# Performance work log

Hardware: AMD Instinct MI355X
Metric: run time of the kernel (lower is better)

## Reference

```python
import jax, jax.numpy as jnp
import numpy as np

D = 16      # stroke_embedding_dim
H = 2       # num_heads
DH = D // H # head dim = 8
HID = 32    # hidden_dim
OUT = 32    # output_dim
N = 250000  # num edge nodes
F = 500000  # num faces
E = 4       # edges per face


def setup_inputs() -> dict:
    key = jax.random.key(0)
    ks = jax.random.split(key, 10)
    s = 1.0 / np.sqrt(D)
    return {
        "node_embed": jax.random.normal(ks[0], (1, N, D), dtype=jnp.float32),
        "face_edge_ids": jax.random.randint(ks[1], (F, E), 0, N),
        # nn.MultiheadAttention in_proj (packed q,k,v) and out_proj, stored [in, out]
        "w_in": jax.random.uniform(ks[2], (D, 3 * D), jnp.float32, -s, s),
        "b_in": jnp.zeros((3 * D,), jnp.float32),
        "w_out": jax.random.uniform(ks[3], (D, D), jnp.float32, -s, s),
        "b_out": jnp.zeros((D,), jnp.float32),
        # fc: Linear(16 -> 32), fc_output: Linear(32 -> 32)
        "fc_w": jax.random.uniform(ks[4], (D, HID), jnp.float32, -s, s),
        "fc_b": jax.random.uniform(ks[5], (HID,), jnp.float32, -s, s),
        "fco_w": jax.random.uniform(ks[6], (HID, OUT), jnp.float32, -1 / np.sqrt(HID), 1 / np.sqrt(HID)),
        "fco_b": jax.random.uniform(ks[7], (OUT,), jnp.float32, -1 / np.sqrt(HID), 1 / np.sqrt(HID)),
    }


def reference(node_embed, face_edge_ids, w_in, b_in, w_out, b_out, fc_w, fc_b, fco_w, fco_b):
    # Gather per-face edge embeddings: [F, E, D]
    x = node_embed[0][face_edge_ids]
    # Packed qkv projection
    qkv = x @ w_in + b_in                                  # [F, E, 3D]
    q, k, v = jnp.split(qkv, 3, axis=-1)
    def heads(t):
        return t.reshape(F, E, H, DH).transpose(0, 2, 1, 3)  # [F, H, E, DH]
    q, k, v = heads(q), heads(k), heads(v)
    scores = jnp.einsum("fhqd,fhkd->fhqk", q, k) / np.sqrt(DH)
    attn = jax.nn.softmax(scores, axis=-1)
    o = jnp.einsum("fhqk,fhkd->fhqd", attn, v)             # [F, H, E, DH]
    o = o.transpose(0, 2, 1, 3).reshape(F, E, D)
    attn_out = o @ w_out + b_out                           # [F, E, D]
    h = jax.nn.relu(attn_out @ fc_w + fc_b)                # [F, E, HID]
    pooled = h.mean(axis=1)                                # [F, HID]
    out = pooled @ fco_w + fco_b                           # [F, OUT]
    return out[None]                                       # [1, F, OUT]
```

## Files before the change

### kernel.cpp

```cpp
#include <hip/hip_runtime.h>
#include <stdint.h>


typedef _Float16 v2h __attribute__((ext_vector_type(2)));
typedef __fp16 h4 __attribute__((ext_vector_type(4)));
typedef float f32x4 __attribute__((ext_vector_type(4)));
typedef uint32_t u32x2 __attribute__((ext_vector_type(2)));

#define DPP_ROT1 0x39
#define DPP_ROT2 0x4E
#define DPP_ROT3 0x93

template<int CTRL>
static __device__ __forceinline__ float dppf(float x) {
    return __builtin_bit_cast(float,
        __builtin_amdgcn_mov_dpp(__builtin_bit_cast(int, x), CTRL, 0xF, 0xF, true));
}

static __device__ __forceinline__ v2h pkh(float a, float b) {
    v2h r; r.x = (_Float16)a; r.y = (_Float16)b; return r;
}
static __device__ __forceinline__ v2h pkrtz(float a, float b) {
#if __has_builtin(__builtin_amdgcn_cvt_pkrtz)
    return __builtin_bit_cast(v2h, __builtin_amdgcn_cvt_pkrtz(a, b));
#else
    return pkh(a, b);
#endif
}
static __device__ __forceinline__ uint32_t bcu(v2h h) {
    return __builtin_bit_cast(uint32_t, h);
}
static __device__ __forceinline__ h4 mkh4(uint32_t lo, uint32_t hi) {
    u32x2 t; t.x = lo; t.y = hi; return __builtin_bit_cast(h4, t);
}
static __device__ __forceinline__ h4 ld2h(const uint32_t* p) {
    u32x2 t; t.x = p[0]; t.y = p[1]; return __builtin_bit_cast(h4, t);
}
static __device__ __forceinline__ f32x4 mfma16(h4 a, h4 b, f32x4 c) {
    return __builtin_amdgcn_mfma_f32_16x16x16f16(a, b, c, 0, 0, 0);
}
static __device__ __forceinline__ h4 packC(f32x4 c) {
    return mkh4(bcu(pkrtz(c[0], c[1])), bcu(pkrtz(c[2], c[3])));
}
static __device__ __forceinline__ h4 packCrelu(f32x4 c) {
    return mkh4(bcu(pkrtz(fmaxf(c[0], 0.f), fmaxf(c[1], 0.f))),
                bcu(pkrtz(fmaxf(c[2], 0.f), fmaxf(c[3], 0.f))));
}
static __device__ __forceinline__ h4 selh(bool keep, h4 x) {
    u32x2 t = __builtin_bit_cast(u32x2, x);
    u32x2 r; r.x = keep ? t.x : 0u; r.y = keep ? t.y : 0u;
    return __builtin_bit_cast(h4, r);
}

__global__ void fold_w(const float* __restrict__ w_in,
                       const float* __restrict__ w_out,
                       const float* __restrict__ b_out,
                       const float* __restrict__ fc_w,
                       const float* __restrict__ fc_b,
                       const float* __restrict__ fco_w,
                       uint32_t* __restrict__ wsu) {
    const int tid = threadIdx.x;
    if (blockIdx.x == 0) {
        if (tid < 384) {
            const int T = tid >> 7, r = tid & 127, l = r >> 1, d = r & 1;
            const int o = 16 * T + (l & 15), k0 = 4 * (l >> 4) + 2 * d;
            wsu[tid] = bcu(pkh(w_in[k0 * 48 + o], w_in[(k0 + 1) * 48 + o]));
        } else if (tid < 640) {
            const int i = tid - 384, b = i >> 7, r = i & 127, l = r >> 1, d = r & 1;
            const int c = 16 * b + (l & 15), k0 = 4 * (l >> 4) + 2 * d;
            float a0 = 0.f, a1 = 0.f;
#pragma unroll
            for (int e = 0; e < 16; ++e) {
                a0 = fmaf(w_out[k0 * 16 + e],       fc_w[e * 32 + c], a0);
                a1 = fmaf(w_out[(k0 + 1) * 16 + e], fc_w[e * 32 + c], a1);
            }
            wsu[tid] = bcu(pkh(a0, a1));
        }
    } else {
        if (tid < 32) {
            float acc = fc_b[tid];
#pragma unroll
            for (int e = 0; e < 16; ++e)
                acc = fmaf(b_out[e], fc_w[e * 32 + tid], acc);
            reinterpret_cast<float*>(wsu)[640 + tid] = acc;
        } else if (tid < 544) {
            const int i = tid - 32;
            const int kt = i >> 8, n = (i >> 7) & 1, r = i & 127, l = r >> 1, d = r & 1;
            const int col = 16 * n + (l & 15), k0 = 16 * kt + 4 * (l >> 4) + 2 * d;
            wsu[672 + i] = bcu(pkh(fco_w[k0 * 32 + col] * 0.25f,
                                   fco_w[(k0 + 1) * 32 + col] * 0.25f));
        }
    }
}

__launch_bounds__(256, 8)
__global__ void face_net(const float* __restrict__ node,
                         const int*   __restrict__ fids,
                         const float* __restrict__ b_in,
                         const uint32_t* __restrict__ wsu,
                         const float* __restrict__ fco_b,
                         float* __restrict__ out, int F) {
    const int l   = threadIdx.x & 63;
    const int wid = threadIdx.x >> 6;
    const int token_base = blockIdx.x * 256 + wid * 64;
    const int total = 4 * F;
    if (token_base >= total) return;
    const int c0 = l & 15, g2 = l >> 4;

    h4 X[4];
#pragma unroll
    for (int a = 0; a < 4; ++a) {
        int tok = token_base + 16 * a + c0;
        tok = tok < total ? tok : total - 1;
        const int nid = fids[tok];
        const float4 xv = *reinterpret_cast<const float4*>(
            node + (size_t)nid * 16 + g2 * 4);
        X[a] = mkh4(bcu(pkrtz(xv.x, xv.y)), bcu(pkrtz(xv.z, xv.w)));
    }

    const h4 WqT  = ld2h(wsu + 0   + l * 2);
    const h4 WkT  = ld2h(wsu + 128 + l * 2);
    const h4 WvB  = ld2h(wsu + 256 + l * 2);
    const h4 EhA0 = ld2h(wsu + 384 + l * 2);
    const h4 EhA1 = ld2h(wsu + 512 + l * 2);
    const h4 Ef00 = ld2h(wsu + 672 + 0 * 128 + l * 2);
    const h4 Ef01 = ld2h(wsu + 672 + 1 * 128 + l * 2);
    const h4 Ef10 = ld2h(wsu + 672 + 2 * 128 + l * 2);
    const h4 Ef11 = ld2h(wsu + 672 + 3 * 128 + l * 2);

    const float4 bq4 = *reinterpret_cast<const float4*>(b_in + 4 * g2);
    const float  bv  = b_in[32 + c0];
    const float* b1f = reinterpret_cast<const float*>(wsu) + 640;
    const float4 b10 = *reinterpret_cast<const float4*>(b1f + 4 * g2);
    const float4 b11 = *reinterpret_cast<const float4*>(b1f + 16 + 4 * g2);
    const float fb0s = fco_b[c0];
    const float fb1s = fco_b[16 + c0];

    const bool scoreH0 = (g2 < 2);
    const bool pvH0    = (c0 < 8);
    const bool valid   = (g2 == (c0 >> 2));
    const int fbase = token_base >> 2;
    const float C = 0.51006974841f;
    const f32x4 zz = {0.f, 0.f, 0.f, 0.f};

#pragma unroll
    for (int a = 0; a < 4; ++a) {
        f32x4 cq = {bq4.x, bq4.y, bq4.z, bq4.w};
        f32x4 cv = {bv, bv, bv, bv};
        const f32x4 Dq = mfma16(WqT, X[a], cq);
        const f32x4 Dk = mfma16(WkT, X[a], zz);
        const f32x4 Dv = mfma16(X[a], WvB, cv);
        const h4 qB = packC(Dq);
        const h4 kA = packC(Dk);
        const h4 vA = packC(Dv);

        const f32x4 S0 = mfma16(selh(scoreH0,  kA), qB, zz);
        const f32x4 S1 = mfma16(selh(!scoreH0, kA), qB, zz);

        const float e00 = __builtin_amdgcn_exp2f(S0[0] * C);
        const float e01 = __builtin_amdgcn_exp2f(S0[1] * C);
        const float e02 = __builtin_amdgcn_exp2f(S0[2] * C);
        const float e03 = __builtin_amdgcn_exp2f(S0[3] * C);
        const float e10 = __builtin_amdgcn_exp2f(S1[0] * C);
        const float e11 = __builtin_amdgcn_exp2f(S1[1] * C);
        const float e12 = __builtin_amdgcn_exp2f(S1[2] * C);
        const float e13 = __builtin_amdgcn_exp2f(S1[3] * C);
        const float r0 = __builtin_amdgcn_rcpf((e00 + e01) + (e02 + e03));
        const float r1 = __builtin_amdgcn_rcpf((e10 + e11) + (e12 + e13));
        const h4 PB0 = selh(valid, mkh4(bcu(pkrtz(e00 * r0, e01 * r0)),
                                        bcu(pkrtz(e02 * r0, e03 * r0))));
        const h4 PB1 = selh(valid, mkh4(bcu(pkrtz(e10 * r1, e11 * r1)),
                                        bcu(pkrtz(e12 * r1, e13 * r1))));

        f32x4 Ot = mfma16(selh(pvH0,  vA), PB0, zz);
        Ot       = mfma16(selh(!pvH0, vA), PB1, Ot);
        const h4 hB = packC(Ot);

        f32x4 ch0 = {b10.x, b10.y, b10.z, b10.w};
        f32x4 ch1 = {b11.x, b11.y, b11.z, b11.w};
        const f32x4 H0 = mfma16(EhA0, hB, ch0);
        const f32x4 H1 = mfma16(EhA1, hB, ch1);

        const h4 AH0 = packCrelu(H0);
        const h4 AH1 = packCrelu(H1);

        const f32x4 O0 = mfma16(AH1, Ef10, mfma16(AH0, Ef00, zz));
        const f32x4 O1 = mfma16(AH1, Ef11, mfma16(AH0, Ef01, zz));
        const float o0 = ((O0[0] + O0[1]) + (O0[2] + O0[3])) + fb0s;
        const float o1 = ((O1[0] + O1[1]) + (O1[2] + O1[3])) + fb1s;

        const float a1 = dppf<DPP_ROT1>(o0);
        const float a2 = dppf<DPP_ROT2>(o0);
        const float a3 = dppf<DPP_ROT3>(o0);
        const float b1 = dppf<DPP_ROT1>(o1);
        const float b2 = dppf<DPP_ROT2>(o1);
        const float b3 = dppf<DPP_ROT3>(o1);
        const int face = fbase + 4 * a + g2;
        if ((c0 & 2) == 0 && face < F) {
            const bool t0 = (c0 & 1) == 0;
            const int q = c0 >> 2;
            const float4 st = make_float4(t0 ? o0 : b3,
                                          t0 ? a1 : o1,
                                          t0 ? a2 : b1,
                                          t0 ? a3 : b2);
            float* ob = out + (size_t)face * 32 + (t0 ? 4 * q : 16 + 4 * q);
            *reinterpret_cast<float4*>(ob) = st;
        }
    }
}

extern "C" void kernel_launch(void* const* d_in, const int* in_sizes, int n_in,
                              void* d_out, int out_size, void* d_ws, size_t ws_size,
                              hipStream_t stream) {
    const float* node  = (const float*)d_in[0];
    const int*   fids  = (const int*)  d_in[1];
    const float* w_in  = (const float*)d_in[2];
    const float* b_in  = (const float*)d_in[3];
    const float* w_out = (const float*)d_in[4];
    const float* b_out = (const float*)d_in[5];
    const float* fc_w  = (const float*)d_in[6];
    const float* fc_b  = (const float*)d_in[7];
    const float* fco_w = (const float*)d_in[8];
    const float* fco_b = (const float*)d_in[9];
    float* out = (float*)d_out;
    uint32_t* wsu = (uint32_t*)d_ws;
    const int F = in_sizes[1] / 4;

    hipLaunchKernelGGL(fold_w, dim3(2), dim3(640), 0, stream,
                       w_in, w_out, b_out, fc_w, fc_b, fco_w, wsu);
    const int threads = F * 4;
    const int blocks = (threads + 255) / 256;
    hipLaunchKernelGGL(face_net, dim3(blocks), dim3(256), 0, stream,
                       node, fids, b_in, wsu, fco_b, out, F);
}
```

Before: 132.8 us.

## Pre-convert node table to fp16 and interleave two tokens per MFMA chain

New measurement: 134.5 us. No clear change (+1.3%).

```diff
diff --git a/kernel.cpp b/kernel.cpp
--- a/kernel.cpp
+++ b/kernel.cpp
@@ -93,8 +93,16 @@
     }
 }
 
-__launch_bounds__(256, 8)
+__global__ void cvt_node(const float* __restrict__ node,
+                         uint32_t* __restrict__ nt, int ndw) {
+    const int i = blockIdx.x * 256 + threadIdx.x;
+    if (i < ndw) nt[i] = bcu(pkrtz(node[2 * i], node[2 * i + 1]));
+}
+
+template<bool F16>
+__launch_bounds__(256, 6)
 __global__ void face_net(const float* __restrict__ node,
+                         const uint32_t* __restrict__ nt,
                          const int*   __restrict__ fids,
                          const float* __restrict__ b_in,
                          const uint32_t* __restrict__ wsu,
@@ -113,9 +121,15 @@
         int tok = token_base + 16 * a + c0;
         tok = tok < total ? tok : total - 1;
         const int nid = fids[tok];
-        const float4 xv = *reinterpret_cast<const float4*>(
-            node + (size_t)nid * 16 + g2 * 4);
-        X[a] = mkh4(bcu(pkrtz(xv.x, xv.y)), bcu(pkrtz(xv.z, xv.w)));
+        if constexpr (F16) {
+            const u32x2 xw = *reinterpret_cast<const u32x2*>(
+                nt + (size_t)nid * 8 + g2 * 2);
+            X[a] = __builtin_bit_cast(h4, xw);
+        } else {
+            const float4 xv = *reinterpret_cast<const float4*>(
+                node + (size_t)nid * 16 + g2 * 4);
+            X[a] = mkh4(bcu(pkrtz(xv.x, xv.y)), bcu(pkrtz(xv.z, xv.w)));
+        }
     }
 
     const h4 WqT  = ld2h(wsu + 0   + l * 2);
@@ -142,69 +156,95 @@
     const int fbase = token_base >> 2;
     const float C = 0.51006974841f;
     const f32x4 zz = {0.f, 0.f, 0.f, 0.f};
-
-#pragma unroll
-    for (int a = 0; a < 4; ++a) {
-        f32x4 cq = {bq4.x, bq4.y, bq4.z, bq4.w};
-        f32x4 cv = {bv, bv, bv, bv};
-        const f32x4 Dq = mfma16(WqT, X[a], cq);
-        const f32x4 Dk = mfma16(WkT, X[a], zz);
-        const f32x4 Dv = mfma16(X[a], WvB, cv);
-        const h4 qB = packC(Dq);
-        const h4 kA = packC(Dk);
-        const h4 vA = packC(Dv);
-
-        const f32x4 S0 = mfma16(selh(scoreH0,  kA), qB, zz);
-        const f32x4 S1 = mfma16(selh(!scoreH0, kA), qB, zz);
-
-        const float e00 = __builtin_amdgcn_exp2f(S0[0] * C);
-        const float e01 = __builtin_amdgcn_exp2f(S0[1] * C);
-        const float e02 = __builtin_amdgcn_exp2f(S0[2] * C);
-        const float e03 = __builtin_amdgcn_exp2f(S0[3] * C);
-        const float e10 = __builtin_amdgcn_exp2f(S1[0] * C);
-        const float e11 = __builtin_amdgcn_exp2f(S1[1] * C);
-        const float e12 = __builtin_amdgcn_exp2f(S1[2] * C);
-        const float e13 = __builtin_amdgcn_exp2f(S1[3] * C);
-        const float r0 = __builtin_amdgcn_rcpf((e00 + e01) + (e02 + e03));
-        const float r1 = __builtin_amdgcn_rcpf((e10 + e11) + (e12 + e13));
-        const h4 PB0 = selh(valid, mkh4(bcu(pkrtz(e00 * r0, e01 * r0)),
-                                        bcu(pkrtz(e02 * r0, e03 * r0))));
-        const h4 PB1 = selh(valid, mkh4(bcu(pkrtz(e10 * r1, e11 * r1)),
-                                        bcu(pkrtz(e12 * r1, e13 * r1))));
-
-        f32x4 Ot = mfma16(selh(pvH0,  vA), PB0, zz);
-        Ot       = mfma16(selh(!pvH0, vA), PB1, Ot);
-        const h4 hB = packC(Ot);
-
-        f32x4 ch0 = {b10.x, b10.y, b10.z, b10.w};
-        f32x4 ch1 = {b11.x, b11.y, b11.z, b11.w};
-        const f32x4 H0 = mfma16(EhA0, hB, ch0);
-        const f32x4 H1 = mfma16(EhA1, hB, ch1);
-
-        const h4 AH0 = packCrelu(H0);
-        const h4 AH1 = packCrelu(H1);
-
-        const f32x4 O0 = mfma16(AH1, Ef10, mfma16(AH0, Ef00, zz));
-        const f32x4 O1 = mfma16(AH1, Ef11, mfma16(AH0, Ef01, zz));
-        const float o0 = ((O0[0] + O0[1]) + (O0[2] + O0[3])) + fb0s;
-        const float o1 = ((O1[0] + O1[1]) + (O1[2] + O1[3])) + fb1s;
-
-        const float a1 = dppf<DPP_ROT1>(o0);
-        const float a2 = dppf<DPP_ROT2>(o0);
-        const float a3 = dppf<DPP_ROT3>(o0);
-        const float b1 = dppf<DPP_ROT1>(o1);
-        const float b2 = dppf<DPP_ROT2>(o1);
-        const float b3 = dppf<DPP_ROT3>(o1);
-        const int face = fbase + 4 * a + g2;
-        if ((c0 & 2) == 0 && face < F) {
-            const bool t0 = (c0 & 1) == 0;
-            const int q = c0 >> 2;
-            const float4 st = make_float4(t0 ? o0 : b3,
-                                          t0 ? a1 : o1,
-                                          t0 ? a2 : b1,
-                                          t0 ? a3 : b2);
-            float* ob = out + (size_t)face * 32 + (t0 ? 4 * q : 16 + 4 * q);
-            *reinterpret_cast<float4*>(ob) = st;
+    const f32x4 cq = {bq4.x, bq4.y, bq4.z, bq4.w};
+    const f32x4 cv = {bv, bv, bv, bv};
+    const f32x4 ch0 = {b10.x, b10.y, b10.z, b10.w};
+    const f32x4 ch1 = {b11.x, b11.y, b11.z, b11.w};
+
+#pragma unroll
+    for (int ap = 0; ap < 2; ++ap) {
+        f32x4 Dq[2], Dk[2], Dv[2];
+#pragma unroll
+        for (int j = 0; j < 2; ++j) {
+            const h4 x = X[2 * ap + j];
+            Dq[j] = mfma16(WqT, x, cq);
+            Dk[j] = mfma16(WkT, x, zz);
+            Dv[j] = mfma16(x, WvB, cv);
+        }
+        h4 qB[2], kA[2], vA[2];
+#pragma unroll
+        for (int j = 0; j < 2; ++j) {
+            qB[j] = packC(Dq[j]); kA[j] = packC(Dk[j]); vA[j] = packC(Dv[j]);
+        }
+        f32x4 S0[2], S1[2];
+#pragma unroll
+        for (int j = 0; j < 2; ++j) {
+            S0[j] = mfma16(selh(scoreH0,  kA[j]), qB[j], zz);
+            S1[j] = mfma16(selh(!scoreH0, kA[j]), qB[j], zz);
+        }
+        h4 PB0[2], PB1[2];
+#pragma unroll
+        for (int j = 0; j < 2; ++j) {
+            const float e00 = __builtin_amdgcn_exp2f(S0[j][0] * C);
+            const float e01 = __builtin_amdgcn_exp2f(S0[j][1] * C);
+            const float e02 = __builtin_amdgcn_exp2f(S0[j][2] * C);
+            const float e03 = __builtin_amdgcn_exp2f(S0[j][3] * C);
+            const float e10 = __builtin_amdgcn_exp2f(S1[j][0] * C);
+            const float e11 = __builtin_amdgcn_exp2f(S1[j][1] * C);
+            const float e12 = __builtin_amdgcn_exp2f(S1[j][2] * C);
+            const float e13 = __builtin_amdgcn_exp2f(S1[j][3] * C);
+            const float r0 = __builtin_amdgcn_rcpf((e00 + e01) + (e02 + e03));
+            const float r1 = __builtin_amdgcn_rcpf((e10 + e11) + (e12 + e13));
+            PB0[j] = selh(valid, mkh4(bcu(pkrtz(e00 * r0, e01 * r0)),
+                                      bcu(pkrtz(e02 * r0, e03 * r0))));
+            PB1[j] = selh(valid, mkh4(bcu(pkrtz(e10 * r1, e11 * r1)),
+                                      bcu(pkrtz(e12 * r1, e13 * r1))));
+        }
+        f32x4 Ot[2];
+#pragma unroll
+        for (int j = 0; j < 2; ++j) {
+            Ot[j] = mfma16(selh(pvH0,  vA[j]), PB0[j], zz);
+            Ot[j] = mfma16(selh(!pvH0, vA[j]), PB1[j], Ot[j]);
+        }
+        h4 hB[2];
+#pragma unroll
+        for (int j = 0; j < 2; ++j) hB[j] = packC(Ot[j]);
+        f32x4 H0[2], H1[2];
+#pragma unroll
+        for (int j = 0; j < 2; ++j) {
+            H0[j] = mfma16(EhA0, hB[j], ch0);
+            H1[j] = mfma16(EhA1, hB[j], ch1);
+        }
+        f32x4 O0[2], O1[2];
+#pragma unroll
+        for (int j = 0; j < 2; ++j) {
+            const h4 AH0 = packCrelu(H0[j]);
+            const h4 AH1 = packCrelu(H1[j]);
+            O0[j] = mfma16(AH1, Ef10, mfma16(AH0, Ef00, zz));
+            O1[j] = mfma16(AH1, Ef11, mfma16(AH0, Ef01, zz));
+        }
+#pragma unroll
+        for (int j = 0; j < 2; ++j) {
+            const int a = 2 * ap + j;
+            const float o0 = ((O0[j][0] + O0[j][1]) + (O0[j][2] + O0[j][3])) + fb0s;
+            const float o1 = ((O1[j][0] + O1[j][1]) + (O1[j][2] + O1[j][3])) + fb1s;
+            const float a1 = dppf<DPP_ROT1>(o0);
+            const float a2 = dppf<DPP_ROT2>(o0);
+            const float a3 = dppf<DPP_ROT3>(o0);
+            const float b1 = dppf<DPP_ROT1>(o1);
+            const float b2 = dppf<DPP_ROT2>(o1);
+            const float b3 = dppf<DPP_ROT3>(o1);
+            const int face = fbase + 4 * a + g2;
+            if ((c0 & 2) == 0 && face < F) {
+                const bool t0 = (c0 & 1) == 0;
+                const int q = c0 >> 2;
+                const float4 st = make_float4(t0 ? o0 : b3,
+                                              t0 ? a1 : o1,
+                                              t0 ? a2 : b1,
+                                              t0 ? a3 : b2);
+                float* ob = out + (size_t)face * 32 + (t0 ? 4 * q : 16 + 4 * q);
+                *reinterpret_cast<float4*>(ob) = st;
+            }
         }
     }
 }
@@ -225,11 +265,23 @@
     float* out = (float*)d_out;
     uint32_t* wsu = (uint32_t*)d_ws;
     const int F = in_sizes[1] / 4;
+    const int ndw = in_sizes[0] / 2;
+    const size_t need = (2048 + (size_t)ndw) * 4;
+    const bool f16tab = ws_size >= need;
 
     hipLaunchKernelGGL(fold_w, dim3(2), dim3(640), 0, stream,
                        w_in, w_out, b_out, fc_w, fc_b, fco_w, wsu);
+    if (f16tab) {
+        hipLaunchKernelGGL(cvt_node, dim3((ndw + 255) / 256), dim3(256), 0,
+                           stream, node, wsu + 2048, ndw);
+    }
     const int threads = F * 4;
     const int blocks = (threads + 255) / 256;
-    hipLaunchKernelGGL(face_net, dim3(blocks), dim3(256), 0, stream,
-                       node, fids, b_in, wsu, fco_b, out, F);
-}
+    if (f16tab) {
+        hipLaunchKernelGGL((face_net<true>), dim3(blocks), dim3(256), 0, stream,
+                           node, wsu + 2048, fids, b_in, wsu, fco_b, out, F);
+    } else {
+        hipLaunchKernelGGL((face_net<false>), dim3(blocks), dim3(256), 0, stream,
+                           node, wsu, fids, b_in, wsu, fco_b, out, F);
+    }
+}
```
